# Kernel tuning notes

Hardware: AMD Instinct MI355X
Metric: run time of the kernel (lower is better)

## Reference

```python
import jax, jax.numpy as jnp
import numpy as np

H = 16  # num_heads
LN_EPS = 1e-5


def _layernorm(x):
    # parameter-free LayerNorm over last dim (the source module creates no LN params)
    mu = jnp.mean(x, axis=-1, keepdims=True)
    var = jnp.var(x, axis=-1, keepdims=True)
    return (x - mu) / jnp.sqrt(var + LN_EPS)


def setup_inputs() -> dict:
    key = jax.random.key(0)
    B, L, D = 8, 1024, 1024
    ks = jax.random.split(key, 12)
    s = 1.0 / np.sqrt(D)
    s4 = 1.0 / np.sqrt(4 * D)
    return {
        "x": jax.random.normal(ks[0], (B, L, D), dtype=jnp.float32),
        "Wq": jax.random.normal(ks[1], (D, D), dtype=jnp.float32) * s,
        "bq": jnp.zeros((D,), dtype=jnp.float32),
        "Wk": jax.random.normal(ks[2], (D, D), dtype=jnp.float32) * s,
        "bk": jnp.zeros((D,), dtype=jnp.float32),
        "Wv": jax.random.normal(ks[3], (D, D), dtype=jnp.float32) * s,
        "bv": jnp.zeros((D,), dtype=jnp.float32),
        "W1": jax.random.normal(ks[4], (D, 4 * D), dtype=jnp.float32) * s,
        "b1": jnp.zeros((4 * D,), dtype=jnp.float32),
        "W2": jax.random.normal(ks[5], (4 * D, D), dtype=jnp.float32) * s4,
        "b2": jnp.zeros((D,), dtype=jnp.float32),
    }


def reference(x, Wq, bq, Wk, bk, Wv, bv, W1, b1, W2, b2):
    B, L, D = x.shape
    Dh = D // H

    def split(t):  # [B,L,D] -> [B,H,L,Dh]
        return t.reshape(B, L, H, Dh).transpose(0, 2, 1, 3)

    q = split(x @ Wq + bq)
    k = split(x @ Wk + bk)
    v = split(x @ Wv + bv)

    # naive full-score attention, materializes [B,H,L,L]
    score = jnp.einsum("bhld,bhmd->bhlm", q, k) / jnp.sqrt(jnp.float32(Dh))
    attn = jax.nn.softmax(score, axis=-1)
    out = jnp.einsum("bhlm,bhmd->bhld", attn, v)
    out = out.transpose(0, 2, 1, 3).reshape(B, L, D)  # concat heads

    x = _layernorm(x + out)  # dropout = identity (eval)
    ffn = jax.nn.gelu(x @ W1 + b1, approximate=False) @ W2 + b2
    x = _layernorm(x + ffn)
    return x
```

## Files before the change

kernel.cpp:

```cpp
#include <hip/hip_runtime.h>

typedef unsigned short u16;
typedef __attribute__((ext_vector_type(8))) short bf16x8;
typedef __attribute__((ext_vector_type(4))) float f32x4;

#define MFMA16(a, b, c) __builtin_amdgcn_mfma_f32_16x16x32_bf16(a, b, c, 0, 0, 0)

__device__ __forceinline__ float b2f(u16 u) {
    unsigned int x = ((unsigned int)u) << 16;
    return __builtin_bit_cast(float, x);
}
__device__ __forceinline__ u16 f2b(float f) {
    unsigned int u = __builtin_bit_cast(unsigned int, f);
    u = u + 0x7fffu + ((u >> 16) & 1u);
    return (u16)(u >> 16);
}
__device__ __forceinline__ u16 f2b_hi(float f) {
    return (u16)(__builtin_bit_cast(unsigned int, f) >> 16);
}
__device__ __forceinline__ float gelu_t(float x) {
    float xc = fminf(fmaxf(x, -8.f), 8.f);
    float tt = __builtin_amdgcn_exp2f(xc * (2.3022077f + 0.1029483f * xc * xc));
    return x * tt * __builtin_amdgcn_rcpf(1.f + tt);
}
__device__ __forceinline__ void gload_lds16(const u16* g, u16* lds) {
    __builtin_amdgcn_global_load_lds(
        (const __attribute__((address_space(1))) unsigned int*)g,
        (__attribute__((address_space(3))) unsigned int*)lds, 16, 0, 0);
}
__device__ __forceinline__ void barrier_raw() {
    asm volatile("" ::: "memory");
    __builtin_amdgcn_s_barrier();
    asm volatile("" ::: "memory");
}
__device__ __forceinline__ void swz_block(int& mb, int& nb) {
    const int NX = gridDim.x;
    const int nwg = NX * gridDim.y;
    const int wg = blockIdx.y * NX + blockIdx.x;
    const int q = nwg >> 3, rmd = nwg & 7;
    const int xcd = wg & 7, idx = wg >> 3;
    const int swz = (xcd < rmd ? xcd * (q + 1) : rmd * (q + 1) + (xcd - rmd) * q) + idx;
    mb = swz / NX;
    nb = swz - mb * NX;
}

__global__ __launch_bounds__(256) void cvt_f2b_kernel(
    const float* __restrict__ in, u16* __restrict__ out, int n)
{
    const int i = (blockIdx.x * 256 + threadIdx.x) * 4;
    if (i >= n) return;
    float4 v = *(const float4*)&in[i];
    ushort4 o;
    o.x = f2b(v.x); o.y = f2b(v.y); o.z = f2b(v.z); o.w = f2b(v.w);
    *(ushort4*)&out[i] = o;
}

__global__ __launch_bounds__(256) void transpose_cvt(
    const float* __restrict__ in, u16* __restrict__ out, int R, int C)
{
    __shared__ u16 tile[64][65];
    const int t = threadIdx.x;
    const int r0 = blockIdx.y * 64, c0 = blockIdx.x * 64;
    const int tr = t >> 4, tc = (t & 15) * 4;
#pragma unroll
    for (int p = 0; p < 4; p++) {
        const int rr = tr + p * 16;
        float4 v = *(const float4*)&in[(size_t)(r0 + rr) * C + c0 + tc];
        tile[rr][tc + 0] = f2b(v.x); tile[rr][tc + 1] = f2b(v.y);
        tile[rr][tc + 2] = f2b(v.z); tile[rr][tc + 3] = f2b(v.w);
    }
    __syncthreads();
#pragma unroll
    for (int p = 0; p < 4; p++) {
        const int cc = tr + p * 16;
        ushort4 v;
        v.x = tile[tc + 0][cc]; v.y = tile[tc + 1][cc];
        v.z = tile[tc + 2][cc]; v.w = tile[tc + 3][cc];
        *(ushort4*)&out[(size_t)(c0 + cc) * R + r0 + tc] = v;
    }
}

template <int EPI>
__global__ __launch_bounds__(256, 2) void gemm_bt(
    const u16* __restrict__ A, const u16* __restrict__ Bt,
    const float* __restrict__ bias, u16* __restrict__ C,
    int M, int N, int K)
{
    __shared__ __attribute__((aligned(16))) u16 sA[2][128 * 32];
    __shared__ __attribute__((aligned(16))) u16 sB[2][128 * 32];
    const int t = threadIdx.x;
    const int lane = t & 63, w = t >> 6;
    const int g = lane >> 4, r = lane & 15;
    const int wr = w >> 1, wc = w & 1;
    int mb, nb;
    swz_block(mb, nb);
    const int m0 = mb * 128, n0 = nb * 128;
    const int arow0 = t >> 2;
    const int ake = (t & 3) * 8;
    const int ldsb = w * 512;

    const f32x4 fz = {0.f, 0.f, 0.f, 0.f};
    f32x4 acc[4][4];
#pragma unroll
    for (int i = 0; i < 4; i++)
#pragma unroll
        for (int j = 0; j < 4; j++) acc[i][j] = fz;

#pragma unroll
    for (int it = 0; it < 2; ++it) {
        gload_lds16(&A[(size_t)(m0 + arow0 + it * 64) * K + ake], &sA[0][ldsb + it * 2048]);
        gload_lds16(&Bt[(size_t)(n0 + arow0 + it * 64) * K + ake], &sB[0][ldsb + it * 2048]);
    }
    __syncthreads();

    const int nk = K >> 5;
    for (int kt = 0; kt < nk; ++kt) {
        const int buf = kt & 1;
        if (kt + 1 < nk) {
            const int k0 = (kt + 1) << 5;
#pragma unroll
            for (int it = 0; it < 2; ++it) {
                gload_lds16(&A[(size_t)(m0 + arow0 + it * 64) * K + k0 + ake], &sA[buf ^ 1][ldsb + it * 2048]);
                gload_lds16(&Bt[(size_t)(n0 + arow0 + it * 64) * K + k0 + ake], &sB[buf ^ 1][ldsb + it * 2048]);
            }
        }
        bf16x8 af[4], bfr[4];
#pragma unroll
        for (int i = 0; i < 4; i++)
            af[i] = *(const bf16x8*)&sA[buf][(wr * 64 + i * 16 + r) * 32 + g * 8];
#pragma unroll
        for (int j = 0; j < 4; j++)
            bfr[j] = *(const bf16x8*)&sB[buf][(wc * 64 + j * 16 + r) * 32 + g * 8];
#pragma unroll
        for (int i = 0; i < 4; i++)
#pragma unroll
            for (int j = 0; j < 4; j++)
                acc[i][j] = MFMA16(af[i], bfr[j], acc[i][j]);
        __syncthreads();
    }

#pragma unroll
    for (int i = 0; i < 4; i++) {
#pragma unroll
        for (int j = 0; j < 4; j++) {
            const int col = n0 + wc * 64 + j * 16 + r;
            const float bs = bias[col];
            const int row0 = m0 + wr * 64 + i * 16 + g * 4;
#pragma unroll
            for (int rg = 0; rg < 4; ++rg) {
                float v = acc[i][j][rg] + bs;
                if (EPI == 1) v = gelu_t(v);
                C[(size_t)(row0 + rg) * N + col] = f2b(v);
            }
        }
    }
}

template <int EPI>
__global__ __launch_bounds__(512, 2) void gemm8p(
    const u16* __restrict__ A, const u16* __restrict__ Bt,
    const float* __restrict__ bias, u16* __restrict__ C,
    int M, int N, int K)
{
    __shared__ __attribute__((aligned(16))) u16 As[4][256][32];
    __shared__ __attribute__((aligned(16))) u16 Bs[4][256][32];

    const int t = threadIdx.x;
    const int lane = t & 63;
    const int g = lane >> 4, r = lane & 15;
    const int wid = t >> 6, wm = wid >> 2, wn = wid & 3;
    int mb, nb;
    swz_block(mb, nb);
    const int m0 = mb * 256, n0 = nb * 256;

    const int srow = t >> 2;
    const int sslot = ((t & 3) ^ (srow & 3)) * 8;

    auto stageA = [&](int u) {
        const int slot = u & 3, ks = u << 5;
#pragma unroll
        for (int h = 0; h < 2; ++h)
            gload_lds16(&A[(size_t)(m0 + srow + h * 128) * K + ks + sslot],
                        &As[slot][srow + h * 128][(t & 3) * 8]);
    };
    auto stageB = [&](int u) {
        const int slot = u & 3, ks = u << 5;
#pragma unroll
        for (int h = 0; h < 2; ++h)
            gload_lds16(&Bt[(size_t)(n0 + srow + h * 128) * K + ks + sslot],
                        &Bs[slot][srow + h * 128][(t & 3) * 8]);
    };

    f32x4 acc[8][4];
    const f32x4 fz = {0.f, 0.f, 0.f, 0.f};
#pragma unroll
    for (int i = 0; i < 8; ++i)
#pragma unroll
        for (int j = 0; j < 4; ++j) acc[i][j] = fz;

    const int S = K >> 5;
    stageA(0); stageB(0); stageA(1); stageB(1); stageA(2); stageB(2);

    const int swA = g ^ (r & 3);

    for (int s = 0; s < S; ++s) {
        if (s < S - 2)       asm volatile("s_waitcnt vmcnt(8)" ::: "memory");
        else if (s == S - 2) asm volatile("s_waitcnt vmcnt(4)" ::: "memory");
        else                 asm volatile("s_waitcnt vmcnt(0)" ::: "memory");
        if (s + 3 < S) stageA(s + 3);
        barrier_raw();

        const int slot = s & 3;
        bf16x8 af[8], bf[4];
#pragma unroll
        for (int i = 0; i < 8; ++i)
            af[i] = *(const bf16x8*)&As[slot][wm * 128 + i * 16 + r][swA * 8];
#pragma unroll
        for (int j = 0; j < 4; ++j)
            bf[j] = *(const bf16x8*)&Bs[slot][wn * 64 + j * 16 + r][swA * 8];

        __builtin_amdgcn_s_setprio(1);
#pragma unroll
        for (int i = 0; i < 8; ++i) {
            acc[i][0] = MFMA16(af[i], bf[0], acc[i][0]);
            acc[i][1] = MFMA16(af[i], bf[1], acc[i][1]);
        }
        __builtin_amdgcn_s_setprio(0);
        barrier_raw();

        if (s + 3 < S) stageB(s + 3);
        barrier_raw();
        __builtin_amdgcn_s_setprio(1);
#pragma unroll
        for (int i = 0; i < 8; ++i) {
            acc[i][2] = MFMA16(af[i], bf[2], acc[i][2]);
            acc[i][3] = MFMA16(af[i], bf[3], acc[i][3]);
        }
        __builtin_amdgcn_s_setprio(0);
        barrier_raw();
    }

#pragma unroll
    for (int i = 0; i < 8; ++i) {
        const int row0 = m0 + wm * 128 + i * 16 + g * 4;
#pragma unroll
        for (int j = 0; j < 4; ++j) {
            const int col = n0 + wn * 64 + j * 16 + r;
            const float bs = bias[col];
#pragma unroll
            for (int rg = 0; rg < 4; ++rg) {
                float v = acc[i][j][rg] + bs;
                if (EPI == 1) v = gelu_t(v);
                C[(size_t)(row0 + rg) * N + col] = f2b(v);
            }
        }
    }
}

__global__ __launch_bounds__(256, 2) void gemm_qkv(
    const u16* __restrict__ A, const u16* __restrict__ Bt,
    const float* __restrict__ bq, const float* __restrict__ bk,
    const float* __restrict__ bv,
    u16* __restrict__ Qo, u16* __restrict__ Ko, u16* __restrict__ Vt,
    int M, int K)
{
    __shared__ __attribute__((aligned(16))) u16 sA[2][128 * 32];
    __shared__ __attribute__((aligned(16))) u16 sB[2][128 * 32];
    const int t = threadIdx.x;
    const int lane = t & 63, w = t >> 6;
    const int g = lane >> 4, r = lane & 15;
    const int wr = w >> 1, wc = w & 1;
    int mb, nb;
    swz_block(mb, nb);
    const int m0 = mb * 128, n0 = nb * 128;
    const int arow0 = t >> 2;
    const int ake = (t & 3) * 8;
    const int ldsb = w * 512;

    const f32x4 fz = {0.f, 0.f, 0.f, 0.f};
    f32x4 acc[4][4];
#pragma unroll
    for (int i = 0; i < 4; i++)
#pragma unroll
        for (int j = 0; j < 4; j++) acc[i][j] = fz;

#pragma unroll
    for (int it = 0; it < 2; ++it) {
        gload_lds16(&A[(size_t)(m0 + arow0 + it * 64) * K + ake], &sA[0][ldsb + it * 2048]);
        gload_lds16(&Bt[(size_t)(n0 + arow0 + it * 64) * K + ake], &sB[0][ldsb + it * 2048]);
    }
    __syncthreads();

    const int nk = K >> 5;
    for (int kt = 0; kt < nk; ++kt) {
        const int buf = kt & 1;
        if (kt + 1 < nk) {
            const int k0 = (kt + 1) << 5;
#pragma unroll
            for (int it = 0; it < 2; ++it) {
                gload_lds16(&A[(size_t)(m0 + arow0 + it * 64) * K + k0 + ake], &sA[buf ^ 1][ldsb + it * 2048]);
                gload_lds16(&Bt[(size_t)(n0 + arow0 + it * 64) * K + k0 + ake], &sB[buf ^ 1][ldsb + it * 2048]);
            }
        }
        bf16x8 af[4], bfr[4];
#pragma unroll
        for (int i = 0; i < 4; i++)
            af[i] = *(const bf16x8*)&sA[buf][(wr * 64 + i * 16 + r) * 32 + g * 8];
#pragma unroll
        for (int j = 0; j < 4; j++)
            bfr[j] = *(const bf16x8*)&sB[buf][(wc * 64 + j * 16 + r) * 32 + g * 8];
#pragma unroll
        for (int i = 0; i < 4; i++)
#pragma unroll
            for (int j = 0; j < 4; j++)
                acc[i][j] = MFMA16(af[i], bfr[j], acc[i][j]);
        __syncthreads();
    }

    const int sel = n0 >> 10;
    const float* bias = (sel == 0) ? bq : (sel == 1) ? bk : bv;
#pragma unroll
    for (int i = 0; i < 4; i++) {
#pragma unroll
        for (int j = 0; j < 4; j++) {
            const int col = n0 + wc * 64 + j * 16 + r;
            const int c1 = col & 1023;
            const float bs = bias[c1];
            const int row0 = m0 + wr * 64 + i * 16 + g * 4;
            if (sel < 2) {
                u16* C = sel ? Ko : Qo;
#pragma unroll
                for (int rg = 0; rg < 4; ++rg)
                    C[(size_t)(row0 + rg) * 1024 + c1] = f2b(acc[i][j][rg] + bs);
            } else {
                const int brow = row0 >> 10;
                const int l = row0 & 1023;
                const int vrow = ((brow << 4) + (c1 >> 6)) * 64 + (c1 & 63);
                ushort4 pk;
                pk.x = f2b(acc[i][j][0] + bs);
                pk.y = f2b(acc[i][j][1] + bs);
                pk.z = f2b(acc[i][j][2] + bs);
                pk.w = f2b(acc[i][j][3] + bs);
                *(ushort4*)&Vt[(size_t)vrow * 1024 + l] = pk;
            }
        }
    }
}

__global__ __launch_bounds__(256, 2) void attn_fwd(
    const u16* __restrict__ Q, const u16* __restrict__ Kb,
    const u16* __restrict__ Vt, u16* __restrict__ O)
{
    __shared__ __attribute__((aligned(16))) u16 sK[2][64 * 64];
    __shared__ __attribute__((aligned(16))) u16 sV[2][64 * 64];
    __shared__ __attribute__((aligned(16))) u16 sP[4][32 * 72];
    const int t = threadIdx.x;
    const int lane = t & 63, w = t >> 6;
    const int g = lane >> 4, r = lane & 15;
    const int bh = blockIdx.y;
    const int b = bh >> 4, h = bh & 15;
    const int q0 = blockIdx.x * 128;
    const size_t tokbase = (size_t)b << 10;
    const float SC = 0.125f * 1.44269504f;

    bf16x8 qf[2][2];
#pragma unroll
    for (int i = 0; i < 2; i++)
#pragma unroll
        for (int c = 0; c < 2; c++)
            qf[i][c] = *(const bf16x8*)&Q[((tokbase + q0 + w * 32 + i * 16 + r) << 10) + h * 64 + c * 32 + g * 8];

    const f32x4 fz = {0.f, 0.f, 0.f, 0.f};
    f32x4 acc[2][4];
    float lrow[2][4];
#pragma unroll
    for (int i = 0; i < 2; i++) {
#pragma unroll
        for (int j = 0; j < 4; j++) acc[i][j] = fz;
#pragma unroll
        for (int rg = 0; rg < 4; rg++) lrow[i][rg] = 0.f;
    }

    const int srow0 = t >> 3;
    const int skesw = ((t & 7) ^ ((t >> 3) & 7)) * 8;
    const int ldsb = w * 512;
    auto stageKV = [&](int kt, int bufsel) {
#pragma unroll
        for (int it = 0; it < 2; ++it) {
            const int row = srow0 + it * 32;
            gload_lds16(&Kb[((tokbase + kt * 64 + row) << 10) + h * 64 + skesw], &sK[bufsel][ldsb + it * 2048]);
            gload_lds16(&Vt[(((size_t)bh * 64 + row) << 10) + kt * 64 + skesw], &sV[bufsel][ldsb + it * 2048]);
        }
    };

    stageKV(0, 0);
    __syncthreads();

    for (int kt = 0; kt < 16; ++kt) {
        const int buf = kt & 1;
        if (kt < 15) stageKV(kt + 1, buf ^ 1);

        f32x4 s[2][4];
#pragma unroll
        for (int i = 0; i < 2; i++)
#pragma unroll
            for (int j = 0; j < 4; j++) s[i][j] = fz;
#pragma unroll
        for (int c = 0; c < 2; c++) {
            bf16x8 kf[4];
#pragma unroll
            for (int j = 0; j < 4; j++)
                kf[j] = *(const bf16x8*)&sK[buf][(j * 16 + r) * 64 + (((c * 4 + g) ^ (r & 7)) * 8)];
#pragma unroll
            for (int i = 0; i < 2; i++)
#pragma unroll
                for (int j = 0; j < 4; j++)
                    s[i][j] = MFMA16(qf[i][c], kf[j], s[i][j]);
        }

#pragma unroll
        for (int i = 0; i < 2; i++) {
#pragma unroll
            for (int rg = 0; rg < 4; rg++) {
                float p0 = __builtin_amdgcn_exp2f(s[i][0][rg] * SC);
                float p1 = __builtin_amdgcn_exp2f(s[i][1][rg] * SC);
                float p2 = __builtin_amdgcn_exp2f(s[i][2][rg] * SC);
                float p3 = __builtin_amdgcn_exp2f(s[i][3][rg] * SC);
                lrow[i][rg] += (p0 + p1) + (p2 + p3);
                const int prow = (i * 16 + g * 4 + rg) * 72;
                sP[w][prow + 0 * 16 + r] = f2b_hi(p0);
                sP[w][prow + 1 * 16 + r] = f2b_hi(p1);
                sP[w][prow + 2 * 16 + r] = f2b_hi(p2);
                sP[w][prow + 3 * 16 + r] = f2b_hi(p3);
            }
        }

#pragma unroll
        for (int c = 0; c < 2; c++) {
            bf16x8 pa[2], vb[4];
#pragma unroll
            for (int i = 0; i < 2; i++)
                pa[i] = *(const bf16x8*)&sP[w][(i * 16 + r) * 72 + c * 32 + g * 8];
#pragma unroll
            for (int j = 0; j < 4; j++)
                vb[j] = *(const bf16x8*)&sV[buf][(j * 16 + r) * 64 + (((c * 4 + g) ^ (r & 7)) * 8)];
#pragma unroll
            for (int i = 0; i < 2; i++)
#pragma unroll
                for (int j = 0; j < 4; j++)
                    acc[i][j] = MFMA16(pa[i], vb[j], acc[i][j]);
        }
        __syncthreads();
    }

#pragma unroll
    for (int i = 0; i < 2; i++)
#pragma unroll
        for (int rg = 0; rg < 4; rg++) {
            float l = lrow[i][rg];
            l += __shfl_xor(l, 1);
            l += __shfl_xor(l, 2);
            l += __shfl_xor(l, 4);
            l += __shfl_xor(l, 8);
            lrow[i][rg] = 1.0f / l;
        }
#pragma unroll
    for (int i = 0; i < 2; i++)
#pragma unroll
        for (int j = 0; j < 4; j++)
#pragma unroll
            for (int rg = 0; rg < 4; rg++) {
                const size_t row = tokbase + q0 + w * 32 + i * 16 + g * 4 + rg;
                const int col = h * 64 + j * 16 + r;
                O[(row << 10) + col] = f2b(acc[i][j][rg] * lrow[i][rg]);
            }
}

template <int FP32OUT>
__global__ __launch_bounds__(256) void resln(
    const u16* __restrict__ a, const u16* __restrict__ bsrc, void* __restrict__ optr)
{
    const int row = blockIdx.x, t = threadIdx.x;
    const size_t base = (size_t)row << 10;
    ushort4 va = *(const ushort4*)&a[base + t * 4];
    ushort4 vb = *(const ushort4*)&bsrc[base + t * 4];
    float v0 = b2f(va.x) + b2f(vb.x);
    float v1 = b2f(va.y) + b2f(vb.y);
    float v2 = b2f(va.z) + b2f(vb.z);
    float v3 = b2f(va.w) + b2f(vb.w);
    float s = v0 + v1 + v2 + v3;
    float ss = v0 * v0 + v1 * v1 + v2 * v2 + v3 * v3;
#pragma unroll
    for (int m = 1; m < 64; m <<= 1) { s += __shfl_xor(s, m); ss += __shfl_xor(ss, m); }
    __shared__ float rs[4], rq[4];
    const int w = t >> 6;
    if ((t & 63) == 0) { rs[w] = s; rq[w] = ss; }
    __syncthreads();
    s = rs[0] + rs[1] + rs[2] + rs[3];
    ss = rq[0] + rq[1] + rq[2] + rq[3];
    const float mu = s * (1.0f / 1024.0f);
    const float var = ss * (1.0f / 1024.0f) - mu * mu;
    const float ri = rsqrtf(var + 1e-5f);
    if (FP32OUT) {
        float4 vo;
        vo.x = (v0 - mu) * ri; vo.y = (v1 - mu) * ri;
        vo.z = (v2 - mu) * ri; vo.w = (v3 - mu) * ri;
        *(float4*)&((float*)optr)[base + t * 4] = vo;
    } else {
        ushort4 vo;
        vo.x = f2b((v0 - mu) * ri); vo.y = f2b((v1 - mu) * ri);
        vo.z = f2b((v2 - mu) * ri); vo.w = f2b((v3 - mu) * ri);
        *(ushort4*)&((u16*)optr)[base + t * 4] = vo;
    }
}

extern "C" void kernel_launch(void* const* d_in, const int* in_sizes, int n_in,
                              void* d_out, int out_size, void* d_ws, size_t ws_size,
                              hipStream_t stream)
{
    (void)in_sizes; (void)n_in; (void)out_size; (void)ws_size;
    const float* x  = (const float*)d_in[0];
    const float* Wq = (const float*)d_in[1];
    const float* bq = (const float*)d_in[2];
    const float* Wk = (const float*)d_in[3];
    const float* bk = (const float*)d_in[4];
    const float* Wv = (const float*)d_in[5];
    const float* bv = (const float*)d_in[6];
    const float* W1 = (const float*)d_in[7];
    const float* b1 = (const float*)d_in[8];
    const float* W2 = (const float*)d_in[9];
    const float* b2 = (const float*)d_in[10];
    float* out = (float*)d_out;
    char* ws = (char*)d_ws;
    const size_t MB = 1u << 20;
    u16* Qb     = (u16*)(ws + 0 * MB);
    u16* Kbf    = (u16*)(ws + 16 * MB);
    u16* Vt     = (u16*)(ws + 32 * MB);
    u16* Ob     = (u16*)(ws + 48 * MB);
    u16* xb     = (u16*)(ws + 64 * MB);
    u16* X1     = (u16*)(ws + 80 * MB);
    u16* W1T    = (u16*)(ws + 96 * MB);
    u16* WqkvT  = (u16*)(ws + 104 * MB);
    u16* W2T    = (u16*)(ws + 104 * MB);
    u16* Hb     = (u16*)(ws + 0 * MB);
    u16* H2     = (u16*)(ws + 64 * MB);

    dim3 blk(256);
    cvt_f2b_kernel<<<dim3(8192), blk, 0, stream>>>(x, xb, 8192 * 1024);
    transpose_cvt<<<dim3(16, 16), blk, 0, stream>>>(Wq, WqkvT, 1024, 1024);
    transpose_cvt<<<dim3(16, 16), blk, 0, stream>>>(Wk, WqkvT + 1024 * 1024, 1024, 1024);
    transpose_cvt<<<dim3(16, 16), blk, 0, stream>>>(Wv, WqkvT + 2048 * 1024, 1024, 1024);
    transpose_cvt<<<dim3(64, 16), blk, 0, stream>>>(W1, W1T, 1024, 4096);

    gemm_qkv<<<dim3(24, 64), blk, 0, stream>>>(xb, WqkvT, bq, bk, bv,
                                               Qb, Kbf, Vt, 8192, 1024);

    transpose_cvt<<<dim3(16, 64), blk, 0, stream>>>(W2, W2T, 4096, 1024);

    attn_fwd<<<dim3(8, 128), blk, 0, stream>>>(Qb, Kbf, Vt, Ob);

    resln<0><<<dim3(8192), blk, 0, stream>>>(xb, Ob, X1);

    gemm8p<1><<<dim3(16, 32), dim3(512), 0, stream>>>(X1, W1T, b1, Hb, 8192, 4096, 1024);
    gemm_bt<0><<<dim3(8, 64), blk, 0, stream>>>(Hb, W2T, b2, H2, 8192, 1024, 4096);

    resln<1><<<dim3(8192), blk, 0, stream>>>(X1, H2, out);
}
```

Measured before the change: 369.6 us.

## Double-buffer LDS fragments in FFN1 GEMM and make K a template constant

```diff
diff --git a/kernel.cpp b/kernel.cpp
--- a/kernel.cpp
+++ b/kernel.cpp
@@ -156,12 +156,13 @@
     }
 }
 
-template <int EPI>
+template <int K, int EPI>
 __global__ __launch_bounds__(512, 2) void gemm8p(
     const u16* __restrict__ A, const u16* __restrict__ Bt,
     const float* __restrict__ bias, u16* __restrict__ C,
-    int M, int N, int K)
-{
+    int M, int N)
+{
+    constexpr int S = K >> 5;
     __shared__ __attribute__((aligned(16))) u16 As[4][256][32];
     __shared__ __attribute__((aligned(16))) u16 Bs[4][256][32];
 
@@ -176,15 +177,12 @@
     const int srow = t >> 2;
     const int sslot = ((t & 3) ^ (srow & 3)) * 8;
 
-    auto stageA = [&](int u) {
+    auto stageAB = [&](int u) {
         const int slot = u & 3, ks = u << 5;
 #pragma unroll
         for (int h = 0; h < 2; ++h)
             gload_lds16(&A[(size_t)(m0 + srow + h * 128) * K + ks + sslot],
                         &As[slot][srow + h * 128][(t & 3) * 8]);
-    };
-    auto stageB = [&](int u) {
-        const int slot = u & 3, ks = u << 5;
 #pragma unroll
         for (int h = 0; h < 2; ++h)
             gload_lds16(&Bt[(size_t)(n0 + srow + h * 128) * K + ks + sslot],
@@ -198,26 +196,35 @@
 #pragma unroll
         for (int j = 0; j < 4; ++j) acc[i][j] = fz;
 
-    const int S = K >> 5;
-    stageA(0); stageB(0); stageA(1); stageB(1); stageA(2); stageB(2);
+    stageAB(0); stageAB(1); stageAB(2);
+    asm volatile("s_waitcnt vmcnt(8)" ::: "memory");
+    barrier_raw();
 
     const int swA = g ^ (r & 3);
-
+    bf16x8 af[8], bf[4];
+#pragma unroll
+    for (int i = 0; i < 8; ++i)
+        af[i] = *(const bf16x8*)&As[0][wm * 128 + i * 16 + r][swA * 8];
+#pragma unroll
+    for (int j = 0; j < 4; ++j)
+        bf[j] = *(const bf16x8*)&Bs[0][wn * 64 + j * 16 + r][swA * 8];
+
+#pragma unroll
     for (int s = 0; s < S; ++s) {
-        if (s < S - 2)       asm volatile("s_waitcnt vmcnt(8)" ::: "memory");
-        else if (s == S - 2) asm volatile("s_waitcnt vmcnt(4)" ::: "memory");
-        else                 asm volatile("s_waitcnt vmcnt(0)" ::: "memory");
-        if (s + 3 < S) stageA(s + 3);
-        barrier_raw();
-
-        const int slot = s & 3;
-        bf16x8 af[8], bf[4];
-#pragma unroll
-        for (int i = 0; i < 8; ++i)
-            af[i] = *(const bf16x8*)&As[slot][wm * 128 + i * 16 + r][swA * 8];
-#pragma unroll
-        for (int j = 0; j < 4; ++j)
-            bf[j] = *(const bf16x8*)&Bs[slot][wn * 64 + j * 16 + r][swA * 8];
+        bf16x8 afn[8], bfn[4];
+        if (s < S - 1) {
+            if (s < S - 2) asm volatile("s_waitcnt vmcnt(4)" ::: "memory");
+            else           asm volatile("s_waitcnt vmcnt(0)" ::: "memory");
+            if (s + 3 < S) stageAB(s + 3);
+            barrier_raw();
+            const int nslot = (s + 1) & 3;
+#pragma unroll
+            for (int i = 0; i < 8; ++i)
+                afn[i] = *(const bf16x8*)&As[nslot][wm * 128 + i * 16 + r][swA * 8];
+#pragma unroll
+            for (int j = 0; j < 4; ++j)
+                bfn[j] = *(const bf16x8*)&Bs[nslot][wn * 64 + j * 16 + r][swA * 8];
+        }
 
         __builtin_amdgcn_s_setprio(1);
 #pragma unroll
@@ -225,19 +232,22 @@
             acc[i][0] = MFMA16(af[i], bf[0], acc[i][0]);
             acc[i][1] = MFMA16(af[i], bf[1], acc[i][1]);
         }
-        __builtin_amdgcn_s_setprio(0);
-        barrier_raw();
-
-        if (s + 3 < S) stageB(s + 3);
-        barrier_raw();
-        __builtin_amdgcn_s_setprio(1);
 #pragma unroll
         for (int i = 0; i < 8; ++i) {
             acc[i][2] = MFMA16(af[i], bf[2], acc[i][2]);
             acc[i][3] = MFMA16(af[i], bf[3], acc[i][3]);
         }
         __builtin_amdgcn_s_setprio(0);
-        barrier_raw();
+
+        if (s < S - 1) {
+            asm volatile("s_waitcnt lgkmcnt(0)" ::: "memory");
+            __builtin_amdgcn_sched_barrier(0);
+            barrier_raw();
+#pragma unroll
+            for (int i = 0; i < 8; ++i) af[i] = afn[i];
+#pragma unroll
+            for (int j = 0; j < 4; ++j) bf[j] = bfn[j];
+        }
     }
 
 #pragma unroll
@@ -561,7 +571,7 @@
 
     resln<0><<<dim3(8192), blk, 0, stream>>>(xb, Ob, X1);
 
-    gemm8p<1><<<dim3(16, 32), dim3(512), 0, stream>>>(X1, W1T, b1, Hb, 8192, 4096, 1024);
+    gemm8p<1024, 1><<<dim3(16, 32), dim3(512), 0, stream>>>(X1, W1T, b1, Hb, 8192, 4096);
     gemm_bt<0><<<dim3(8, 64), blk, 0, stream>>>(Hb, W2T, b2, H2, 8192, 1024, 4096);
 
     resln<1><<<dim3(8192), blk, 0, stream>>>(X1, H2, out);
```

Measured after the change: 358.2 us. 1.03x faster.
